# Kernel tuning notes

Measured on AMD Instinct MI355X. Metric: run time of the kernel, lower is better.

## Reference

```python
import jax, jax.numpy as jnp
import numpy as np

IMG = 800.0        # image size (square)
STRIDE = 16        # backbone stride
PRE = 6000         # pre-NMS proposals (test_before_rpn_proposal_num)
POST = 300         # post-NMS proposals (test_after_rpn_proposal_num)
OUT = 7            # RoIAlign output size
SR = 2             # sampling ratio (fixed stand-in for adaptive -1)
NMS_THR = 0.7      # rpn_nms_thr_iou
MIN_SIZE = 16.0    # rpn_min_size
NCLS = 21          # num_classes + background
NEG = -1e30


def xywh2xyxy(b):
    return jnp.concatenate([b[..., :2], b[..., :2] + b[..., 2:]], -1)


def iou_one_vs_all(box, boxes):
    x1 = jnp.maximum(box[0], boxes[:, 0]); y1 = jnp.maximum(box[1], boxes[:, 1])
    x2 = jnp.minimum(box[2], boxes[:, 2]); y2 = jnp.minimum(box[3], boxes[:, 3])
    inter = jnp.maximum(x2 - x1, 0.0) * jnp.maximum(y2 - y1, 0.0)
    a = (box[2] - box[0]) * (box[3] - box[1])
    b = (boxes[:, 2] - boxes[:, 0]) * (boxes[:, 3] - boxes[:, 1])
    return inter / (a + b - inter + 1e-9)


def nms(boxes, scores, thr, k):
    # Greedy NMS with a fixed number of kept boxes (jit-static shapes).
    boxes = jax.lax.stop_gradient(boxes)
    scores = jax.lax.stop_gradient(scores)
    n = scores.shape[0]
    idx = jnp.arange(n)

    def step(sc, _):
        best = jnp.argmax(sc)
        ious = iou_one_vs_all(boxes[best], boxes)
        sc = jnp.where((ious > thr) | (idx == best), NEG, sc)
        return sc, best

    _, keep = jax.lax.scan(step, scores, None, length=k)
    return keep  # [k] int32 indices


def roi_align(feat, rois_xyxy, scale, out, sr):
    # feat [C,H,W], rois_xyxy [K,4] in image coords -> [K,C,out,out]
    C, H, W = feat.shape
    K = rois_xyxy.shape[0]
    x1 = rois_xyxy[:, 0] * scale; y1 = rois_xyxy[:, 1] * scale
    x2 = rois_xyxy[:, 2] * scale; y2 = rois_xyxy[:, 3] * scale
    bw = (x2 - x1) / out; bh = (y2 - y1) / out
    grid = jnp.arange(out, dtype=jnp.float32)
    sub = (jnp.arange(sr, dtype=jnp.float32) + 0.5) / sr
    xs = x1[:, None, None] + (grid[None, :, None] + sub[None, None, :]) * bw[:, None, None]  # [K,out,sr]
    ys = y1[:, None, None] + (grid[None, :, None] + sub[None, None, :]) * bh[:, None, None]
    shp = (K, out, out, sr, sr)  # [K, oy, ox, sy, sx]
    xg = jnp.broadcast_to(xs[:, None, :, None, :], shp)
    yg = jnp.broadcast_to(ys[:, :, None, :, None], shp)
    x0 = jnp.floor(xg); y0 = jnp.floor(yg)
    wx = xg - x0; wy = yg - y0
    x0i = jnp.clip(x0.astype(jnp.int32), 0, W - 1); x1i = jnp.clip(x0i + 1, 0, W - 1)
    y0i = jnp.clip(y0.astype(jnp.int32), 0, H - 1); y1i = jnp.clip(y0i + 1, 0, H - 1)
    v00 = feat[:, y0i, x0i]  # [C,K,out,out,sr,sr]
    v01 = feat[:, y0i, x1i]
    v10 = feat[:, y1i, x0i]
    v11 = feat[:, y1i, x1i]
    wx = wx[None]; wy = wy[None]
    val = v00 * (1 - wy) * (1 - wx) + v01 * (1 - wy) * wx + v10 * wy * (1 - wx) + v11 * wy * wx
    pooled = val.mean(axis=(-1, -2))  # [C,K,out,out]
    return jnp.transpose(pooled, (1, 0, 2, 3))


def _forward(feat, proposals, scores, fc1_w, fc1_b, fc2_w, fc2_b, cls_w, cls_b, reg_w, reg_b):
    std = jnp.tile(jnp.array([0.1, 0.1, 0.2, 0.2], jnp.float32), NCLS)  # target_std per class

    def per_image(fb, pr, sc):
        # mark small proposals as ignored (score -> -inf), as in forward
        sc = jnp.where((pr[:, 2] < MIN_SIZE) | (pr[:, 3] < MIN_SIZE), NEG, sc)
        tsc, tid = jax.lax.top_k(sc, PRE)
        tb = pr[tid]                       # [PRE,4] xywh
        txyxy = xywh2xyxy(tb)
        keep = nms(txyxy, tsc, NMS_THR, POST)
        sb = tb[keep]                      # [POST,4] xywh
        sxyxy = txyxy[keep]
        rf = roi_align(fb, sxyxy, 1.0 / STRIDE, OUT, SR)   # [POST,512,7,7]
        x = rf.reshape(POST, -1)
        x = jax.nn.relu(x @ fc1_w + fc1_b)
        x = jax.nn.relu(x @ fc2_w + fc2_b)
        cls = x @ cls_w + cls_b            # [POST,21]
        reg = (x @ reg_w + reg_b) * std    # reg * target_std + target_mean(=0)
        reg = reg.reshape(POST, NCLS, 4)
        # proposal2bbox: xy = p_xy + d_xy*p_wh ; wh = p_wh * exp(d_wh)
        xy = sb[:, None, :2] + reg[..., :2] * sb[:, None, 2:]
        wh = sb[:, None, 2:] * jnp.exp(reg[..., 2:])
        dec = jnp.clip(jnp.concatenate([xy, xy + wh], -1), 0.0, IMG)
        return jnp.concatenate([jax.nn.softmax(cls, -1), dec.reshape(POST, NCLS * 4)], -1)

    return jax.vmap(per_image)(feat, proposals, scores)  # [B, POST, 21 + 84]


def setup_inputs() -> dict:
    key = jax.random.key(0)
    ks = jax.random.split(key, 12)
    B, C, H, W = 1, 512, 50, 50
    N = 22500  # 50*50*9 anchors
    feat = jax.random.normal(ks[0], (B, C, H, W), jnp.float32)
    xy = jax.random.uniform(ks[1], (B, N, 2), jnp.float32) * (IMG - 64.0)
    wh = 8.0 + jax.random.uniform(ks[2], (B, N, 2), jnp.float32) * 392.0  # some below min_size=16
    proposals = jnp.concatenate([xy, wh], -1)
    scores = jax.random.uniform(ks[3], (B, N), jnp.float32)
    D = C * OUT * OUT  # 25088
    return {
        "feat": feat,
        "proposals": proposals,
        "scores": scores,
        "fc1_w": jax.random.normal(ks[4], (D, 4096), jnp.float32) * 0.01,
        "fc1_b": jnp.zeros((4096,), jnp.float32),
        "fc2_w": jax.random.normal(ks[5], (4096, 4096), jnp.float32) * 0.01,
        "fc2_b": jnp.zeros((4096,), jnp.float32),
        "cls_w": jax.random.normal(ks[6], (4096, NCLS), jnp.float32) * 0.01,
        "cls_b": jnp.zeros((NCLS,), jnp.float32),
        "reg_w": jax.random.normal(ks[7], (4096, NCLS * 4), jnp.float32) * 0.001,
        "reg_b": jnp.zeros((NCLS * 4,), jnp.float32),
    }


def reference(feat, proposals, scores, fc1_w, fc1_b, fc2_w, fc2_b, cls_w, cls_b, reg_w, reg_b):
    return _forward(feat, proposals, scores, fc1_w, fc1_b, fc2_w, fc2_b, cls_w, cls_b, reg_w, reg_b)
```

## Files before the change

kernel.cpp:

```cpp
#include <hip/hip_runtime.h>
#include <stdint.h>


#define NEGV -1e30f

typedef __attribute__((ext_vector_type(8))) short short8;
typedef __attribute__((ext_vector_type(4))) float f32x4;

__device__ __forceinline__ uint16_t f2bf(float f) {
  uint32_t u = __builtin_bit_cast(uint32_t, f);
  u = (u + 0x7FFFu + ((u >> 16) & 1u)) >> 16;
  return (uint16_t)u;
}
__device__ __forceinline__ float bf2f(uint16_t h) {
  return __builtin_bit_cast(float, ((uint32_t)h) << 16);
}
__device__ __forceinline__ uint32_t fkey(float f) {
  uint32_t u = __builtin_bit_cast(uint32_t, f);
  return (u & 0x80000000u) ? ~u : (u | 0x80000000u);
}

__global__ __launch_bounds__(256) void prep_kernel(
    const float* __restrict__ proposals, const float* __restrict__ scores,
    uint32_t* __restrict__ keys, uint64_t* __restrict__ sortbuf,
    int* __restrict__ counter) {
  int i = blockIdx.x * 256 + threadIdx.x;
  if (i < 8192) sortbuf[i] = 0ULL;
  if (i == 0) *counter = 0;
  if (i < 22500) {
    float w = proposals[i * 4 + 2], h = proposals[i * 4 + 3];
    float s = scores[i];
    s = (w < 16.0f || h < 16.0f) ? NEGV : s;
    keys[i] = fkey(s);
  }
}

__global__ __launch_bounds__(1024) void select_kernel(
    const uint32_t* __restrict__ keys, uint32_t* __restrict__ cutoff) {
  __shared__ uint32_t hist[256];
  __shared__ uint32_t s_prefix;
  __shared__ int s_remaining;
  int tid = threadIdx.x;
  if (tid == 0) { s_prefix = 0; s_remaining = 6000; }
  __syncthreads();
  for (int round = 0; round < 4; round++) {
    int shift = 24 - round * 8;
    for (int i = tid; i < 256; i += 1024) hist[i] = 0;
    __syncthreads();
    uint32_t prefix = s_prefix;
    uint32_t pmask = (round == 0) ? 0u : (0xFFFFFFFFu << (shift + 8));
    for (int i = tid; i < 22500; i += 1024) {
      uint32_t kv = keys[i];
      if ((kv & pmask) == (prefix & pmask))
        atomicAdd(&hist[(kv >> shift) & 255u], 1u);
    }
    __syncthreads();
    if (tid == 0) {
      int rem = s_remaining;
      int chosen = 0;
      for (int b = 255; b >= 0; b--) {
        int c = (int)hist[b];
        if (c >= rem) { chosen = b; break; }
        rem -= c;
      }
      s_prefix = prefix | ((uint32_t)chosen << shift);
      s_remaining = rem;
    }
    __syncthreads();
  }
  if (tid == 0) *cutoff = s_prefix;
}

__global__ __launch_bounds__(256) void compact_kernel(
    const uint32_t* __restrict__ keys, const uint32_t* __restrict__ cutoff,
    uint64_t* __restrict__ sortbuf, int* __restrict__ counter) {
  int i = blockIdx.x * 256 + threadIdx.x;
  if (i >= 22500) return;
  uint32_t kv = keys[i];
  if (kv >= *cutoff) {
    int p = atomicAdd(counter, 1);
    if (p < 8192)
      sortbuf[p] = ((uint64_t)kv << 32) | (uint32_t)(~(uint32_t)i);
  }
}

__global__ __launch_bounds__(1024) void sort_kernel(
    const uint64_t* __restrict__ sortbuf, int* __restrict__ sorted_idx) {
  __shared__ uint64_t v[8192];
  int tid = threadIdx.x;
  for (int i = tid; i < 8192; i += 1024) v[i] = sortbuf[i];
  __syncthreads();
  for (int k = 2; k <= 8192; k <<= 1) {
    for (int j = k >> 1; j > 0; j >>= 1) {
      for (int i = tid; i < 8192; i += 1024) {
        int ixj = i ^ j;
        if (ixj > i) {
          uint64_t a = v[i], b = v[ixj];
          bool up = (i & k) == 0;
          if (up ? (a < b) : (a > b)) { v[i] = b; v[ixj] = a; }
        }
      }
      __syncthreads();
    }
  }
  for (int i = tid; i < 6000; i += 1024)
    sorted_idx[i] = (int)(~(uint32_t)(v[i] & 0xFFFFFFFFull));
}

__global__ __launch_bounds__(256) void gather_kernel(
    const float* __restrict__ proposals, const int* __restrict__ sorted_idx,
    float4* __restrict__ sxyxy, float4* __restrict__ sxywh) {
  int i = blockIdx.x * 256 + threadIdx.x;
  if (i >= 6000) return;
  int oi = sorted_idx[i];
  float x = proposals[oi * 4 + 0], y = proposals[oi * 4 + 1];
  float w = proposals[oi * 4 + 2], h = proposals[oi * 4 + 3];
  sxywh[i] = make_float4(x, y, w, h);
  sxyxy[i] = make_float4(x, y, x + w, y + h);
}

__global__ __launch_bounds__(256) void ioumat_kernel(
    const float4* __restrict__ boxes, uint32_t* __restrict__ M) {
#pragma clang fp contract(off)
  int idx = blockIdx.x * 256 + threadIdx.x;
  if (idx >= 6000 * 188) return;
  int j = idx / 188;
  int w = idx - j * 188;
  float4 bb = boxes[j];
  float ba = (bb.z - bb.x) * (bb.w - bb.y);
  int base = w * 32;
  int lim = min(6000 - base, 32);
  uint32_t bits = 0;
  for (int b = 0; b < lim; b++) {
    float4 ob = boxes[base + b];
    float xx1 = fmaxf(bb.x, ob.x);
    float yy1 = fmaxf(bb.y, ob.y);
    float xx2 = fminf(bb.z, ob.z);
    float yy2 = fminf(bb.w, ob.w);
    float inter = fmaxf(xx2 - xx1, 0.0f) * fmaxf(yy2 - yy1, 0.0f);
    float oa = (ob.z - ob.x) * (ob.w - ob.y);
    float iou = inter / (ba + oa - inter + 1e-9f);
    if (iou > 0.7f) bits |= (1u << b);
  }
  M[idx] = bits;
}

__global__ __launch_bounds__(256) void nms_reduce_kernel(
    const uint32_t* __restrict__ M, const float4* __restrict__ sxyxy,
    const float4* __restrict__ sxywh, float4* __restrict__ keep_xyxy,
    float4* __restrict__ keep_xywh) {
  __shared__ uint32_t remv[188];
  __shared__ int keeps[300];
  __shared__ int s_ck[64];
  __shared__ int s_nk, s_nck;
  int tid = threadIdx.x;
  if (tid < 188) remv[tid] = (tid == 187) ? 0xFFFF0000u : 0u;
  if (tid == 0) { s_nk = 0; s_nck = 0; }
  __syncthreads();
  for (int c = 0; c < 94; c++) {
    if (tid < 64) {
      int row = c * 64 + tid;
      uint32_t lo = 0, hi = 0;
      if (row < 6000) {
        lo = M[(size_t)row * 188 + 2 * c];
        hi = M[(size_t)row * 188 + 2 * c + 1];
      }
      uint64_t alive =
          ~(((uint64_t)remv[2 * c + 1] << 32) | (uint64_t)remv[2 * c]);
      int nk = s_nk;
      int nck = 0;
      while (alive != 0 && nk < 300) {
        int b = (int)__builtin_ctzll(alive);
        int j = c * 64 + b;
        if (tid == 0) { keeps[nk] = j; s_ck[nck] = j; }
        nk++;
        nck++;
        uint64_t rb = ((uint64_t)(uint32_t)__shfl((int)hi, b, 64) << 32) |
                      (uint64_t)(uint32_t)__shfl((int)lo, b, 64);
        alive &= ~rb;
        alive &= ~(1ull << b);
      }
      if (tid == 0) { s_nk = nk; s_nck = nck; }
    }
    __syncthreads();
    int nck = s_nck;
    for (int i = tid; i < nck * 188; i += 256) {
      int r = i / 188;
      int wd = i - r * 188;
      atomicOr(&remv[wd], M[(size_t)s_ck[r] * 188 + wd]);
    }
    __syncthreads();
    if (s_nk >= 300) break;
  }
  __syncthreads();
  int nk = s_nk;
  for (int i = tid; i < 300; i += 256) {
    int kp = (i < nk) ? keeps[i] : 0;
    keep_xyxy[i] = sxyxy[kp];
    keep_xywh[i] = sxywh[kp];
  }
}

__global__ __launch_bounds__(256) void roi_kernel(
    const float* __restrict__ feat, const float4* __restrict__ keep_xyxy,
    uint16_t* __restrict__ A) {
  int r = blockIdx.x;
  int tid = threadIdx.x;
  uint16_t* out = A + (size_t)r * 25088;
  if (r >= 300) {
    for (int k = tid; k < 25088; k += 256) out[k] = 0;
    return;
  }
  __shared__ int xi0[14], xi1[14], yi0[14], yi1[14];
  __shared__ float wxs[14], wys[14];
  if (tid < 28) {
    int axis = tid / 14;
    int t = tid % 14;
    int g = t >> 1, sxi = t & 1;
    float4 box = keep_xyxy[r];
    float lo = (axis ? box.y : box.x) * 0.0625f;
    float hi = (axis ? box.w : box.z) * 0.0625f;
    float bsz = (hi - lo) / 7.0f;
    float sub = ((float)sxi + 0.5f) * 0.5f;
    float coord = lo + ((float)g + sub) * bsz;
    float f = floorf(coord);
    float frac = coord - f;
    int i0 = (int)f;
    i0 = min(max(i0, 0), 49);
    int i1 = min(i0 + 1, 49);
    if (axis == 0) { xi0[t] = i0; xi1[t] = i1; wxs[t] = frac; }
    else           { yi0[t] = i0; yi1[t] = i1; wys[t] = frac; }
  }
  __syncthreads();
  for (int k = tid; k < 25088; k += 256) {
    int c = k / 49;
    int pos = k - c * 49;
    int py = pos / 7, px = pos - py * 7;
    const float* fc = feat + (size_t)c * 2500;
    float val = 0.0f;
#pragma unroll
    for (int sy = 0; sy < 2; sy++) {
      int iy = py * 2 + sy;
      float wy = wys[iy];
      int y0 = yi0[iy], y1 = yi1[iy];
#pragma unroll
      for (int sx = 0; sx < 2; sx++) {
        int ix = px * 2 + sx;
        float wx = wxs[ix];
        int x0 = xi0[ix], x1 = xi1[ix];
        float v00 = fc[y0 * 50 + x0], v01 = fc[y0 * 50 + x1];
        float v10 = fc[y1 * 50 + x0], v11 = fc[y1 * 50 + x1];
        val += v00 * (1.0f - wy) * (1.0f - wx) + v01 * (1.0f - wy) * wx +
               v10 * wy * (1.0f - wx) + v11 * wy * wx;
      }
    }
    out[k] = f2bf(val * 0.25f);
  }
}

#define MTILES 5
#define NTILES 4
__global__ __launch_bounds__(256) void gemm_kernel(
    const uint16_t* __restrict__ A, const float* __restrict__ W,
    float* __restrict__ P, int K, int S) {
  __shared__ uint16_t As[320 * 32];
  __shared__ uint16_t Bs[64 * 40];
  const int nb = blockIdx.x;
  const int s = blockIdx.y;
  const int kchunk = K / S;
  const int steps = kchunk >> 5;
  const int k0base = s * kchunk;
  const int tid = threadIdx.x;
  const int w = tid >> 6;
  const int l = tid & 63;
  const int q = l >> 4;
  const int l15 = l & 15;

  f32x4 acc[MTILES][NTILES];
#pragma unroll
  for (int i = 0; i < MTILES; i++)
#pragma unroll
    for (int j = 0; j < NTILES; j++) acc[i][j] = (f32x4)0.0f;

  const int ng = (tid & 15) << 2;
  const int kp = tid >> 4;

  for (int kk = 0; kk < steps; kk++) {
    const int k0 = k0base + (kk << 5);
#pragma unroll
    for (int t = 0; t < 5; t++) {
      int cidx = w * 320 + t * 64 + l;
      int m = cidx >> 2;
      int co = (cidx & 3) << 3;
      const uint16_t* gp = A + (size_t)m * K + k0 + co;
      __builtin_amdgcn_global_load_lds(
          (const __attribute__((address_space(1))) void*)gp,
          (__attribute__((address_space(3))) void*)(As + (w * 320 + t * 64) * 8),
          16, 0, 0);
    }
    {
      const float* wp = W + (size_t)(k0 + 2 * kp) * 4096 + nb * 64 + ng;
      f32x4 f0 = *(const f32x4*)wp;
      f32x4 f1 = *(const f32x4*)(wp + 4096);
#pragma unroll
      for (int j = 0; j < 4; j++) {
        uint32_t v = (uint32_t)f2bf(f0[j]) | ((uint32_t)f2bf(f1[j]) << 16);
        *(uint32_t*)&Bs[(ng + j) * 40 + 2 * kp] = v;
      }
    }
    __syncthreads();
    short8 bfr[NTILES];
#pragma unroll
    for (int nt = 0; nt < NTILES; nt++)
      bfr[nt] = *(const short8*)&Bs[(nt * 16 + l15) * 40 + q * 8];
#pragma unroll
    for (int mt = 0; mt < MTILES; mt++) {
      int mrow = (w * MTILES + mt) * 16 + l15;
      short8 afr = *(const short8*)&As[mrow * 32 + q * 8];
#pragma unroll
      for (int nt = 0; nt < NTILES; nt++)
        acc[mt][nt] =
            __builtin_amdgcn_mfma_f32_16x16x32_bf16(afr, bfr[nt], acc[mt][nt], 0, 0, 0);
    }
    __syncthreads();
  }
#pragma unroll
  for (int mt = 0; mt < MTILES; mt++)
#pragma unroll
    for (int nt = 0; nt < NTILES; nt++)
#pragma unroll
      for (int r = 0; r < 4; r++) {
        int m = (w * MTILES + mt) * 16 + q * 4 + r;
        int n = nb * 64 + nt * 16 + l15;
        P[((size_t)s * 320 + m) * 4096 + n] = acc[mt][nt][r];
      }
}

__global__ __launch_bounds__(256) void reduce_kernel(
    const float* __restrict__ P, const float* __restrict__ bias,
    uint16_t* __restrict__ X) {
  int i = blockIdx.x * 256 + threadIdx.x;
  if (i >= 320 * 4096) return;
  int n = i & 4095;
  float s = 0.0f;
#pragma unroll
  for (int j = 0; j < 8; j++) s += P[(size_t)j * 320 * 4096 + i];
  s += bias[n];
  s = fmaxf(s, 0.0f);
  X[i] = f2bf(s);
}

__global__ __launch_bounds__(256) void headw_kernel(
    const float* __restrict__ cls_w, const float* __restrict__ reg_w,
    uint16_t* __restrict__ Wh) {
  int i = blockIdx.x * 256 + threadIdx.x;
  if (i >= 112 * 4096) return;
  int n = i >> 12, k = i & 4095;
  float v = 0.0f;
  if (n < 21) v = cls_w[k * 21 + n];
  else if (n < 105) v = reg_w[k * 84 + (n - 21)];
  Wh[i] = f2bf(v);
}

#define HNT 7
__global__ __launch_bounds__(256) void headgemm_kernel(
    const uint16_t* __restrict__ X3, const uint16_t* __restrict__ Wh,
    float* __restrict__ HP) {
  const int s = blockIdx.x;
  const int tid = threadIdx.x;
  const int w = tid >> 6, l = tid & 63, q = l >> 4, l15 = l & 15;
  f32x4 acc[MTILES][HNT];
#pragma unroll
  for (int i = 0; i < MTILES; i++)
#pragma unroll
    for (int j = 0; j < HNT; j++) acc[i][j] = (f32x4)0.0f;
#pragma unroll 4
  for (int kk = 0; kk < 16; kk++) {
    int k0 = s * 512 + kk * 32 + q * 8;
    short8 bfr[HNT];
#pragma unroll
    for (int nt = 0; nt < HNT; nt++)
      bfr[nt] = *(const short8*)(Wh + (size_t)(nt * 16 + l15) * 4096 + k0);
#pragma unroll
    for (int mt = 0; mt < MTILES; mt++) {
      short8 afr =
          *(const short8*)(X3 + (size_t)((w * MTILES + mt) * 16 + l15) * 4096 + k0);
#pragma unroll
      for (int nt = 0; nt < HNT; nt++)
        acc[mt][nt] =
            __builtin_amdgcn_mfma_f32_16x16x32_bf16(afr, bfr[nt], acc[mt][nt], 0, 0, 0);
    }
  }
#pragma unroll
  for (int mt = 0; mt < MTILES; mt++)
#pragma unroll
    for (int nt = 0; nt < HNT; nt++)
#pragma unroll
      for (int r = 0; r < 4; r++) {
        int m = (w * MTILES + mt) * 16 + q * 4 + r;
        int n = nt * 16 + l15;
        HP[((size_t)s * 320 + m) * 112 + n] = acc[mt][nt][r];
      }
}

__global__ __launch_bounds__(128) void head_epi_kernel(
    const float* __restrict__ HP, const float* __restrict__ cls_b,
    const float* __restrict__ reg_b, const float4* __restrict__ keep_xywh,
    float* __restrict__ out) {
  int m = blockIdx.x;
  int tid = threadIdx.x;
  __shared__ float row[112];
  if (tid < 105) {
    float v = 0.0f;
#pragma unroll
    for (int s = 0; s < 8; s++) v += HP[((size_t)s * 320 + m) * 112 + tid];
    if (tid < 21) {
      v += cls_b[tid];
    } else {
      int j = tid - 21;
      v += reg_b[j];
      v *= ((j & 3) < 2) ? 0.1f : 0.2f;
    }
    row[tid] = v;
  }
  __syncthreads();
  if (tid < 105) {
    float val;
    if (tid < 21) {
      float mx = row[0];
      for (int j = 1; j < 21; j++) mx = fmaxf(mx, row[j]);
      float sum = 0.0f;
      for (int j = 0; j < 21; j++) sum += expf(row[j] - mx);
      val = expf(row[tid] - mx) / sum;
    } else {
      int j = tid - 21;
      int comp = j & 3;
      int cls = j >> 2;
      float r0 = row[21 + cls * 4 + 0];
      float r1 = row[21 + cls * 4 + 1];
      float r2 = row[21 + cls * 4 + 2];
      float r3 = row[21 + cls * 4 + 3];
      float4 sb = keep_xywh[m];
      float x = sb.x + r0 * sb.z;
      float y = sb.y + r1 * sb.w;
      if (comp == 0) val = x;
      else if (comp == 1) val = y;
      else if (comp == 2) val = x + sb.z * expf(r2);
      else val = y + sb.w * expf(r3);
      val = fminf(fmaxf(val, 0.0f), 800.0f);
    }
    out[(size_t)m * 105 + tid] = val;
  }
}

extern "C" void kernel_launch(void* const* d_in, const int* in_sizes, int n_in,
                              void* d_out, int out_size, void* d_ws, size_t ws_size,
                              hipStream_t stream) {
  const float* feat      = (const float*)d_in[0];
  const float* proposals = (const float*)d_in[1];
  const float* scores    = (const float*)d_in[2];
  const float* fc1_w     = (const float*)d_in[3];
  const float* fc1_b     = (const float*)d_in[4];
  const float* fc2_w     = (const float*)d_in[5];
  const float* fc2_b     = (const float*)d_in[6];
  const float* cls_w     = (const float*)d_in[7];
  const float* cls_b     = (const float*)d_in[8];
  const float* reg_w     = (const float*)d_in[9];
  const float* reg_b     = (const float*)d_in[10];
  float* out = (float*)d_out;

  char* ws = (char*)d_ws;
  size_t off = 0;
  auto alloc = [&](size_t bytes) -> void* {
    void* p = ws + off;
    off = (off + bytes + 255) & ~(size_t)255;
    return p;
  };
  uint32_t* keys      = (uint32_t*)alloc(22500 * 4);
  int*      misc      = (int*)alloc(256);
  uint64_t* sortbuf   = (uint64_t*)alloc(8192 * 8);
  int*      sorted_idx= (int*)alloc(6000 * 4);
  float4*   sxyxy     = (float4*)alloc(6000 * 16);
  float4*   sxywh     = (float4*)alloc(6000 * 16);
  float4*   keep_xyxy = (float4*)alloc(300 * 16);
  float4*   keep_xywh = (float4*)alloc(300 * 16);
  uint16_t* Abuf      = (uint16_t*)alloc((size_t)320 * 25088 * 2);
  uint16_t* X2        = (uint16_t*)alloc((size_t)320 * 4096 * 2);
  uint16_t* X3        = (uint16_t*)alloc((size_t)320 * 4096 * 2);
  uint16_t* Wh        = (uint16_t*)alloc((size_t)112 * 4096 * 2);
  float*    HP        = (float*)alloc((size_t)8 * 320 * 112 * 4);
  float*    partials  = (float*)alloc((size_t)8 * 320 * 4096 * 4);
  uint32_t* cutoff    = (uint32_t*)misc;
  int*      counter   = misc + 1;
  uint32_t* M = (uint32_t*)partials;

  prep_kernel<<<88, 256, 0, stream>>>(proposals, scores, keys, sortbuf, counter);
  select_kernel<<<1, 1024, 0, stream>>>(keys, cutoff);
  compact_kernel<<<88, 256, 0, stream>>>(keys, cutoff, sortbuf, counter);
  sort_kernel<<<1, 1024, 0, stream>>>(sortbuf, sorted_idx);
  gather_kernel<<<24, 256, 0, stream>>>(proposals, sorted_idx, sxyxy, sxywh);
  ioumat_kernel<<<4407, 256, 0, stream>>>(sxyxy, M);
  nms_reduce_kernel<<<1, 256, 0, stream>>>(M, sxyxy, sxywh, keep_xyxy, keep_xywh);
  roi_kernel<<<320, 256, 0, stream>>>(feat, keep_xyxy, Abuf);
  headw_kernel<<<1792, 256, 0, stream>>>(cls_w, reg_w, Wh);
  gemm_kernel<<<dim3(64, 8), 256, 0, stream>>>(Abuf, fc1_w, partials, 25088, 8);
  reduce_kernel<<<5120, 256, 0, stream>>>(partials, fc1_b, X2);
  gemm_kernel<<<dim3(64, 8), 256, 0, stream>>>(X2, fc2_w, partials, 4096, 8);
  reduce_kernel<<<5120, 256, 0, stream>>>(partials, fc2_b, X3);
  headgemm_kernel<<<8, 256, 0, stream>>>(X3, Wh, HP);
  head_epi_kernel<<<300, 128, 0, stream>>>(HP, cls_b, reg_b, keep_xywh, out);
}
```

Before: 1.216 ms.

## Parallelize top-k selection, replace bitonic sort with rank sort, double GEMM splits

The serial histogram scan in select_kernel becomes a parallel suffix-sum, and the single-block bitonic sort is replaced by a 128-block rank-by-counting kernel that scatters each key to its rank. The NMS reduce kernel preloads the diagonal IoU-mask blocks into shared memory before its serial loop. The split-K factor of the FC GEMMs goes from 8 to 16 to fill more CUs, at the cost of a larger partials buffer and a reduce kernel that reads twice as much. The rank approach assumes unique keys, which the index tiebreak provides.

```diff
diff --git a/kernel.cpp b/kernel.cpp
--- a/kernel.cpp
+++ b/kernel.cpp
@@ -3,6 +3,7 @@
 
 
 #define NEGV -1e30f
+#define SPLITS 16
 
 typedef __attribute__((ext_vector_type(8))) short short8;
 typedef __attribute__((ext_vector_type(4))) float f32x4;
@@ -38,6 +39,7 @@
 __global__ __launch_bounds__(1024) void select_kernel(
     const uint32_t* __restrict__ keys, uint32_t* __restrict__ cutoff) {
   __shared__ uint32_t hist[256];
+  __shared__ int ssum[256];
   __shared__ uint32_t s_prefix;
   __shared__ int s_remaining;
   int tid = threadIdx.x;
@@ -45,7 +47,7 @@
   __syncthreads();
   for (int round = 0; round < 4; round++) {
     int shift = 24 - round * 8;
-    for (int i = tid; i < 256; i += 1024) hist[i] = 0;
+    if (tid < 256) hist[tid] = 0;
     __syncthreads();
     uint32_t prefix = s_prefix;
     uint32_t pmask = (round == 0) ? 0u : (0xFFFFFFFFu << (shift + 8));
@@ -55,16 +57,24 @@
         atomicAdd(&hist[(kv >> shift) & 255u], 1u);
     }
     __syncthreads();
-    if (tid == 0) {
-      int rem = s_remaining;
-      int chosen = 0;
-      for (int b = 255; b >= 0; b--) {
-        int c = (int)hist[b];
-        if (c >= rem) { chosen = b; break; }
-        rem -= c;
+    if (tid < 256) ssum[tid] = (int)hist[tid];
+    __syncthreads();
+    for (int offs = 1; offs < 256; offs <<= 1) {
+      int v = 0;
+      if (tid < 256 && tid + offs < 256) v = ssum[tid + offs];
+      __syncthreads();
+      if (tid < 256) ssum[tid] += v;
+      __syncthreads();
+    }
+    int rem = s_remaining;
+    __syncthreads();
+    if (tid < 256) {
+      int s_here = ssum[tid];
+      int s_next = (tid == 255) ? 0 : ssum[tid + 1];
+      if (s_here >= rem && s_next < rem) {
+        s_prefix = prefix | ((uint32_t)tid << shift);
+        s_remaining = rem - s_next;
       }
-      s_prefix = prefix | ((uint32_t)chosen << shift);
-      s_remaining = rem;
     }
     __syncthreads();
   }
@@ -84,27 +94,33 @@
   }
 }
 
-__global__ __launch_bounds__(1024) void sort_kernel(
+__global__ __launch_bounds__(256) void rank_kernel(
     const uint64_t* __restrict__ sortbuf, int* __restrict__ sorted_idx) {
-  __shared__ uint64_t v[8192];
+  __shared__ uint64_t comp[8192];
+  __shared__ int cnt[64];
   int tid = threadIdx.x;
-  for (int i = tid; i < 8192; i += 1024) v[i] = sortbuf[i];
-  __syncthreads();
-  for (int k = 2; k <= 8192; k <<= 1) {
-    for (int j = k >> 1; j > 0; j >>= 1) {
-      for (int i = tid; i < 8192; i += 1024) {
-        int ixj = i ^ j;
-        if (ixj > i) {
-          uint64_t a = v[i], b = v[ixj];
-          bool up = (i & k) == 0;
-          if (up ? (a < b) : (a > b)) { v[i] = b; v[ixj] = a; }
-        }
-      }
-      __syncthreads();
-    }
-  }
-  for (int i = tid; i < 6000; i += 1024)
-    sorted_idx[i] = (int)(~(uint32_t)(v[i] & 0xFFFFFFFFull));
+  for (int i = tid; i < 8192; i += 256) comp[i] = sortbuf[i];
+  if (tid < 64) cnt[tid] = 0;
+  __syncthreads();
+  int il = tid & 63;
+  int sub = tid >> 6;
+  uint64_t my = comp[blockIdx.x * 64 + il];
+  const uint64_t* base = &comp[sub * 2048];
+  int c = 0;
+#pragma unroll 4
+  for (int j = 0; j < 2048; j += 2) {
+    uint64_t a = base[j], b = base[j + 1];
+    c += (a > my) ? 1 : 0;
+    c += (b > my) ? 1 : 0;
+  }
+  atomicAdd(&cnt[il], c);
+  __syncthreads();
+  if (tid < 64) {
+    int rank = cnt[tid];
+    uint64_t m2 = comp[blockIdx.x * 64 + tid];
+    if (m2 != 0ULL && rank < 6000)
+      sorted_idx[rank] = (int)(~(uint32_t)(m2 & 0xFFFFFFFFull));
+  }
 }
 
 __global__ __launch_bounds__(256) void gather_kernel(
@@ -149,22 +165,28 @@
     const uint32_t* __restrict__ M, const float4* __restrict__ sxyxy,
     const float4* __restrict__ sxywh, float4* __restrict__ keep_xyxy,
     float4* __restrict__ keep_xywh) {
+  __shared__ uint64_t diag[94 * 64];
   __shared__ uint32_t remv[188];
   __shared__ int keeps[300];
   __shared__ int s_ck[64];
   __shared__ int s_nk, s_nck;
   int tid = threadIdx.x;
+  for (int t = tid; t < 94 * 64; t += 256) {
+    int c = t >> 6, r = t & 63;
+    int row = c * 64 + r;
+    uint64_t v = 0;
+    if (row < 6000)
+      v = (uint64_t)M[(size_t)row * 188 + 2 * c] |
+          ((uint64_t)M[(size_t)row * 188 + 2 * c + 1] << 32);
+    diag[t] = v;
+  }
   if (tid < 188) remv[tid] = (tid == 187) ? 0xFFFF0000u : 0u;
   if (tid == 0) { s_nk = 0; s_nck = 0; }
   __syncthreads();
   for (int c = 0; c < 94; c++) {
     if (tid < 64) {
-      int row = c * 64 + tid;
-      uint32_t lo = 0, hi = 0;
-      if (row < 6000) {
-        lo = M[(size_t)row * 188 + 2 * c];
-        hi = M[(size_t)row * 188 + 2 * c + 1];
-      }
+      uint64_t myrow = diag[c * 64 + tid];
+      uint32_t lo = (uint32_t)myrow, hi = (uint32_t)(myrow >> 32);
       uint64_t alive =
           ~(((uint64_t)remv[2 * c + 1] << 32) | (uint64_t)remv[2 * c]);
       int nk = s_nk;
@@ -344,7 +366,7 @@
   int n = i & 4095;
   float s = 0.0f;
 #pragma unroll
-  for (int j = 0; j < 8; j++) s += P[(size_t)j * 320 * 4096 + i];
+  for (int j = 0; j < SPLITS; j++) s += P[(size_t)j * 320 * 4096 + i];
   s += bias[n];
   s = fmaxf(s, 0.0f);
   X[i] = f2bf(s);
@@ -489,7 +511,7 @@
   uint16_t* X3        = (uint16_t*)alloc((size_t)320 * 4096 * 2);
   uint16_t* Wh        = (uint16_t*)alloc((size_t)112 * 4096 * 2);
   float*    HP        = (float*)alloc((size_t)8 * 320 * 112 * 4);
-  float*    partials  = (float*)alloc((size_t)8 * 320 * 4096 * 4);
+  float*    partials  = (float*)alloc((size_t)SPLITS * 320 * 4096 * 4);
   uint32_t* cutoff    = (uint32_t*)misc;
   int*      counter   = misc + 1;
   uint32_t* M = (uint32_t*)partials;
@@ -497,15 +519,15 @@
   prep_kernel<<<88, 256, 0, stream>>>(proposals, scores, keys, sortbuf, counter);
   select_kernel<<<1, 1024, 0, stream>>>(keys, cutoff);
   compact_kernel<<<88, 256, 0, stream>>>(keys, cutoff, sortbuf, counter);
-  sort_kernel<<<1, 1024, 0, stream>>>(sortbuf, sorted_idx);
+  rank_kernel<<<128, 256, 0, stream>>>(sortbuf, sorted_idx);
   gather_kernel<<<24, 256, 0, stream>>>(proposals, sorted_idx, sxyxy, sxywh);
   ioumat_kernel<<<4407, 256, 0, stream>>>(sxyxy, M);
   nms_reduce_kernel<<<1, 256, 0, stream>>>(M, sxyxy, sxywh, keep_xyxy, keep_xywh);
   roi_kernel<<<320, 256, 0, stream>>>(feat, keep_xyxy, Abuf);
   headw_kernel<<<1792, 256, 0, stream>>>(cls_w, reg_w, Wh);
-  gemm_kernel<<<dim3(64, 8), 256, 0, stream>>>(Abuf, fc1_w, partials, 25088, 8);
+  gemm_kernel<<<dim3(64, SPLITS), 256, 0, stream>>>(Abuf, fc1_w, partials, 25088, SPLITS);
   reduce_kernel<<<5120, 256, 0, stream>>>(partials, fc1_b, X2);
-  gemm_kernel<<<dim3(64, 8), 256, 0, stream>>>(X2, fc2_w, partials, 4096, 8);
+  gemm_kernel<<<dim3(64, SPLITS), 256, 0, stream>>>(X2, fc2_w, partials, 4096, SPLITS);
   reduce_kernel<<<5120, 256, 0, stream>>>(partials, fc2_b, X3);
   headgemm_kernel<<<8, 256, 0, stream>>>(X3, Wh, HP);
   head_epi_kernel<<<300, 128, 0, stream>>>(HP, cls_b, reg_b, keep_xywh, out);
```

New measurement: 1.165 ms. 1.04x faster.
